# Optimization experiments

Hardware: AMD Instinct MI355X
Metric: run time of the kernel (lower is better)

## Reference

```python
import jax, jax.numpy as jnp
import numpy as np

H = 8  # n_heads

def setup_inputs() -> dict:
    key = jax.random.key(0)
    k1, k2, k3, k4, k5 = jax.random.split(key, 5)
    B, N, D = 4, 2048, 512
    x = jax.random.normal(k1, (B, N, D), dtype=jnp.float32)
    mask_flat = jax.random.randint(k2, (B, N), 0, 2).astype(bool)
    s = 1.0 / np.sqrt(D)
    Wq = jax.random.normal(k3, (D, D), dtype=jnp.float32) * s
    Wkv = jax.random.normal(k4, (D, 2 * D), dtype=jnp.float32) * s
    Wo = jax.random.normal(k5, (D, D), dtype=jnp.float32) * s
    return {"x": x, "mask_flat": mask_flat, "Wq": Wq, "Wkv": Wkv, "Wo": Wo}

def reference(x, mask_flat, Wq, Wkv, Wo):
    B, N, D = x.shape
    d = D // H
    scale = d ** -0.5
    kv = x @ Wkv                                   # (B,N,2D)
    k, v = jnp.split(kv, 2, axis=-1)
    q = x @ Wq                                     # (B,N,D)
    # (B,H,N,d)
    q = q.reshape(B, N, H, d).transpose(0, 2, 1, 3)
    k = k.reshape(B, N, H, d).transpose(0, 2, 1, 3)
    v = v.reshape(B, N, H, d).transpose(0, 2, 1, 3)
    attn = jax.nn.softmax(jnp.einsum('bhmd,bhnd->bhmn', q, k) * scale, axis=-1)
    res = jnp.einsum('bhmn,bhnd->bhmd', attn, v)   # (B,H,N,d)
    out = res.transpose(0, 2, 1, 3).reshape(B, N, D) @ Wo
    # non-masked query positions produce zero output (residual elsewhere keeps them)
    return jnp.where(mask_flat[..., None], out, 0.0)
```

## Files before the change

kernel.cpp:

```cpp
#include <hip/hip_runtime.h>

typedef __bf16 bf16x8 __attribute__((ext_vector_type(8)));
typedef float f32x4 __attribute__((ext_vector_type(4)));
typedef float f32x16 __attribute__((ext_vector_type(16)));
typedef unsigned short u16x8 __attribute__((ext_vector_type(8)));
typedef unsigned int u32x4 __attribute__((ext_vector_type(4)));
typedef int i32x2 __attribute__((ext_vector_type(2)));

__device__ inline unsigned short f2bf(float f) {
    __bf16 h = (__bf16)f;
    return __builtin_bit_cast(unsigned short, h);
}

__device__ inline unsigned int pkbf(float lo, float hi) {
    return (unsigned int)f2bf(lo) | ((unsigned int)f2bf(hi) << 16);
}

__device__ inline float fexp2(float x) {
#if __has_builtin(__builtin_amdgcn_exp2f)
    return __builtin_amdgcn_exp2f(x);
#else
    return exp2f(x);
#endif
}

__device__ inline f32x4 mfma16(u16x8 a, u16x8 b, f32x4 c) {
    return __builtin_amdgcn_mfma_f32_16x16x32_bf16(
        __builtin_bit_cast(bf16x8, a), __builtin_bit_cast(bf16x8, b), c, 0, 0, 0);
}

__device__ inline f32x16 mfma32(u16x8 a, u16x8 b, f32x16 c) {
    return __builtin_amdgcn_mfma_f32_32x32x16_bf16(
        __builtin_bit_cast(bf16x8, a), __builtin_bit_cast(bf16x8, b), c, 0, 0, 0);
}

__device__ inline i32x2 permswap(unsigned int a, unsigned int b, int hi) {
#if __has_builtin(__builtin_amdgcn_permlane32_swap)
    (void)hi;
    return __builtin_amdgcn_permlane32_swap((int)a, (int)b, false, false);
#else
    int pa_ = __shfl_xor((int)a, 32);
    int pb_ = __shfl_xor((int)b, 32);
    i32x2 r;
    r[0] = hi ? pb_ : (int)a;
    r[1] = hi ? (int)b : pa_;
    return r;
#endif
}

__device__ inline void gld_lds16(const unsigned short* gsrc, unsigned short* ldst) {
    __builtin_amdgcn_global_load_lds(
        (const __attribute__((address_space(1))) unsigned int*)gsrc,
        (__attribute__((address_space(3))) unsigned int*)ldst, 16, 0, 0);
}

#define WAIT_VM(n)                                          \
    asm volatile("s_waitcnt vmcnt(" #n ")" ::: "memory");   \
    __builtin_amdgcn_sched_barrier(0)
#define WAIT_LGKM0                                          \
    asm volatile("s_waitcnt lgkmcnt(0)" ::: "memory");      \
    __builtin_amdgcn_sched_barrier(0)
#define BARRIER                                             \
    __builtin_amdgcn_s_barrier();                           \
    __builtin_amdgcn_sched_barrier(0)

__global__ __launch_bounds__(256) void cvt_f32_bf16(const float* __restrict__ in,
                                                    unsigned short* __restrict__ out, long n) {
    long i = ((long)blockIdx.x * blockDim.x + threadIdx.x) * 4;
    if (i >= n) return;
    float4 v = *(const float4*)(in + i);
    ushort4 r;
    r.x = f2bf(v.x); r.y = f2bf(v.y); r.z = f2bf(v.z); r.w = f2bf(v.w);
    *(ushort4*)(out + i) = r;
}

__global__ __launch_bounds__(256) void transpose_cvt_tiled(const float* __restrict__ W,
                                                           unsigned short* __restrict__ Wt,
                                                           int K, int N, float scale) {
    __shared__ float tile[64][65];
    const int n0 = blockIdx.x * 64, k0 = blockIdx.y * 64;
    const int c = threadIdx.x & 63;
    const int r4 = threadIdx.x >> 6;
#pragma unroll
    for (int i = 0; i < 16; i++) {
        int r = r4 * 16 + i;
        tile[r][c] = W[(long)(k0 + r) * N + n0 + c];
    }
    __syncthreads();
#pragma unroll
    for (int i = 0; i < 16; i++) {
        int rr = r4 * 16 + i;
        Wt[(long)(n0 + rr) * K + k0 + c] = f2bf(tile[c][rr] * scale);
    }
}

__global__ __launch_bounds__(256) void scan_mask(const int* __restrict__ mask,
                                                 int* __restrict__ idx, int* __restrict__ cnt) {
    const int b = blockIdx.x;
    const int tid = threadIdx.x;
    __shared__ int wsum[4];
    int m[8]; int pc = 0;
#pragma unroll
    for (int k = 0; k < 8; k++) { m[k] = mask[b * 2048 + tid * 8 + k]; pc += (m[k] != 0); }
    int s = pc;
    const int lane = tid & 63;
    for (int off = 1; off < 64; off <<= 1) {
        int v = __shfl_up(s, off);
        if (lane >= off) s += v;
    }
    if (lane == 63) wsum[tid >> 6] = s;
    __syncthreads();
    int wbase = 0;
    for (int w = 0; w < (tid >> 6); w++) wbase += wsum[w];
    int run = wbase + s - pc;
#pragma unroll
    for (int k = 0; k < 8; k++) if (m[k]) idx[b * 2048 + (run++)] = tid * 8 + k;
    if (tid == 255) cnt[b] = wbase + s;
}

template<int WRITE_BF16, int MASKED>
__global__ __launch_bounds__(256) void gemm_bt(const unsigned short* __restrict__ A,
                                               const unsigned short* __restrict__ Bt,
                                               void* __restrict__ Cv,
                                               int M, int N, int K,
                                               const int* __restrict__ mask) {
    __shared__ unsigned short AsL[2][128 * 32];
    __shared__ unsigned short BsL[2][128 * 32];
    const int tid = threadIdx.x;
    const int lane = tid & 63;
    const int wid = tid >> 6;
    const int lg = lane >> 4, lr = lane & 15;
    const int wm = wid >> 1, wn = wid & 1;
    const long m0 = (long)blockIdx.y * 128, n0 = (long)blockIdx.x * 128;

    f32x4 acc[4][4] = {};

    const unsigned short* aS0 = A  + (m0 + (tid >> 2)) * K + (tid & 3) * 8;
    const unsigned short* aS1 = A  + (m0 + 64 + (tid >> 2)) * K + (tid & 3) * 8;
    const unsigned short* bS0 = Bt + (n0 + (tid >> 2)) * K + (tid & 3) * 8;
    const unsigned short* bS1 = Bt + (n0 + 64 + (tid >> 2)) * K + (tid & 3) * 8;

#define GSTAGE(bufi, k0v)                                    \
    {                                                        \
        gld_lds16(aS0 + (k0v), &AsL[bufi][wid * 512]);       \
        gld_lds16(aS1 + (k0v), &AsL[bufi][2048 + wid * 512]);\
        gld_lds16(bS0 + (k0v), &BsL[bufi][wid * 512]);       \
        gld_lds16(bS1 + (k0v), &BsL[bufi][2048 + wid * 512]);\
    }
#define GREAD(cur)                                                                    \
    {                                                                                 \
        _Pragma("unroll")                                                             \
        for (int i = 0; i < 4; i++) {                                                 \
            af[i]  = *(const u16x8*)&AsL[cur][(wm * 64 + i * 16 + lr) * 32 + lg * 8]; \
            bfr[i] = *(const u16x8*)&BsL[cur][(wn * 64 + i * 16 + lr) * 32 + lg * 8]; \
        }                                                                             \
    }
#define GMFMA                                                                  \
    {                                                                          \
        _Pragma("unroll")                                                      \
        for (int i = 0; i < 4; i++)                                            \
            _Pragma("unroll")                                                  \
            for (int j = 0; j < 4; j++)                                        \
                acc[i][j] = mfma16(af[i], bfr[j], acc[i][j]);                  \
    }

    const int nk = K >> 5;
    GSTAGE(0, 0);
    GSTAGE(1, 32);
    for (int t = 0; t < nk - 1; t++) {
        const int cur = t & 1;
        u16x8 af[4], bfr[4];
        WAIT_VM(4);
        BARRIER;
        GREAD(cur);
        WAIT_LGKM0;
        BARRIER;
        if (t < nk - 2) GSTAGE(cur, (t + 2) * 32);
        GMFMA;
    }
    {
        u16x8 af[4], bfr[4];
        WAIT_VM(0);
        BARRIER;
        GREAD((nk - 1) & 1);
        GMFMA;
    }
#undef GSTAGE
#undef GREAD
#undef GMFMA

#pragma unroll
    for (int i = 0; i < 4; i++)
#pragma unroll
        for (int j = 0; j < 4; j++)
#pragma unroll
            for (int r = 0; r < 4; r++) {
                long row = m0 + wm * 64 + i * 16 + lg * 4 + r;
                long col = n0 + wn * 64 + j * 16 + lr;
                float v = acc[i][j][r];
                if (MASKED) {
                    if (!mask[row]) v = 0.0f;
                    ((float*)Cv)[row * N + col] = v;
                } else if (WRITE_BF16) {
                    ((unsigned short*)Cv)[row * N + col] = f2bf(v);
                } else {
                    ((float*)Cv)[row * N + col] = v;
                }
            }
}

__global__ __launch_bounds__(256) void attn_kernel(const unsigned short* __restrict__ qk,
                                                   const unsigned short* __restrict__ vT,
                                                   unsigned short* __restrict__ res,
                                                   const int* __restrict__ idxm,
                                                   const int* __restrict__ cntm) {
    const int Nseq = 2048, LD = 1024;
    const long T = 8192;
    const int id = blockIdx.x;
    const int xcd = id & 7, jj = id >> 3;
    const int g = xcd + 8 * (jj & 3);
    const int qt = jj >> 2;
    const int b = g >> 3, h = g & 7;

    const int count = cntm[b];
    if (qt * 64 >= count) return;

    const int tid = threadIdx.x;
    const int wid = tid >> 6, lane = tid & 63;
    const int qL = lane & 31, hi = lane >> 5;
    const int qh = wid >> 1, kvh = wid & 1;

    __shared__ unsigned short LDSB[4][2][4096];
    unsigned short* myL = &LDSB[wid][0][0];

    const int i_q = qt * 64 + qh * 32 + qL;
    const int gi = idxm[b * 2048 + (i_q < count ? i_q : count - 1)];
    const long qrow = (long)b * Nseq + gi;
    u16x8 qf[4];
#pragma unroll
    for (int j = 0; j < 4; j++)
        qf[j] = *(const u16x8*)(qk + qrow * LD + h * 64 + 16 * j + 8 * hi);

    f32x16 oacc[2] = {};
    f32x16 lacc = {};
    u16x8 onesf;
#pragma unroll
    for (int e = 0; e < 8; e++) onesf[e] = 0x3F80;

    const int R0 = lane >> 3, p0 = lane & 7;
    const unsigned short* kS = qk + 512 + ((long)b * Nseq + kvh * 1024 + R0) * LD + h * 64
                               + ((p0 ^ R0) * 8);
    const int rV = lane >> 2, pV = lane & 3;
    const unsigned short* vS = vT + ((long)h * 64 + rV) * T + (long)b * Nseq + kvh * 1024
                               + ((pV ^ ((lane >> 3) & 3)) * 8);
    const int rsw = qL & 7;

#define STAGE(bufi)                                                          \
    {                                                                        \
        unsigned short* dK = myL + (bufi) * 4096;                            \
        _Pragma("unroll")                                                    \
        for (int i = 0; i < 4; i++)                                          \
            gld_lds16(kS + (long)i * 8 * LD, dK + i * 512);                  \
        _Pragma("unroll")                                                    \
        for (int i = 0; i < 4; i++)                                          \
            gld_lds16(vS + (long)i * 16 * T, dK + 2048 + i * 512);           \
        kS += 32L * LD; vS += 32;                                            \
    }

#define READ_KF(buf)                                                           \
    {                                                                          \
        _Pragma("unroll")                                                      \
        for (int j = 0; j < 4; j++)                                            \
            kf[j] = *(const u16x8*)&myL[(buf) * 4096 + qL * 64                 \
                                        + (((2 * j + hi) ^ rsw) * 8)];         \
    }
#define READ_VF(buf)                                                           \
    {                                                                          \
        _Pragma("unroll")                                                      \
        for (int db = 0; db < 2; db++)                                         \
            _Pragma("unroll")                                                  \
            for (int jk = 0; jk < 2; jk++)                                     \
                vf[db][jk] = *(const u16x8*)&myL[(buf) * 4096 + 2048           \
                                 + (db * 32 + qL) * 32                         \
                                 + (((2 * jk + hi) ^ ((qL >> 1) & 3)) * 8)];   \
    }

#define QKNEXT(SN)                                                             \
    {                                                                          \
        SN = (f32x16){};                                                       \
        _Pragma("unroll")                                                      \
        for (int j = 0; j < 4; j++) SN = mfma32(kf[j], qf[j], SN);             \
    }

#define PACK_PV(SC)                                                                    \
    {                                                                                  \
        unsigned int w[8];                                                             \
        _Pragma("unroll")                                                              \
        for (int i = 0; i < 8; i++)                                                    \
            w[i] = pkbf(fexp2(SC[2 * i]), fexp2(SC[2 * i + 1]));                       \
        u16x8 pa[2];                                                                   \
        _Pragma("unroll")                                                              \
        for (int hh = 0; hh < 2; hh++) {                                               \
            i32x2 ra = permswap(w[4 * hh + 0], w[4 * hh + 2], hi);                     \
            i32x2 rb = permswap(w[4 * hh + 1], w[4 * hh + 3], hi);                     \
            u32x4 fw;                                                                  \
            fw[0] = (unsigned)ra[0]; fw[1] = (unsigned)rb[0];                          \
            fw[2] = (unsigned)ra[1]; fw[3] = (unsigned)rb[1];                          \
            pa[hh] = __builtin_bit_cast(u16x8, fw);                                    \
        }                                                                              \
        _Pragma("unroll")                                                              \
        for (int jk = 0; jk < 2; jk++) {                                               \
            lacc = mfma32(pa[jk], onesf, lacc);                                        \
            oacc[0] = mfma32(pa[jk], vf[0][jk], oacc[0]);                              \
            oacc[1] = mfma32(pa[jk], vf[1][jk], oacc[1]);                              \
        }                                                                              \
    }

#define STEP(SC, SN, cur)                                                      \
    {                                                                          \
        WAIT_VM(4);                                                            \
        READ_VF(cur);                                                          \
        READ_KF(cur ^ 1);                                                      \
        WAIT_LGKM0;                                                            \
        STAGE(cur);                                                            \
        QKNEXT(SN);                                                            \
        PACK_PV(SC);                                                           \
    }

    u16x8 kf[4], vf[2][2];
    f32x16 sA, sB;

    STAGE(0);
    STAGE(1);
    WAIT_VM(12);
    READ_KF(0);
    WAIT_LGKM0;
    QKNEXT(sA);

    for (int t = 0; t < 30; t += 2) {
        STEP(sA, sB, 0);
        STEP(sB, sA, 1);
    }
    {
        WAIT_VM(4);
        READ_VF(0);
        READ_KF(1);
        WAIT_LGKM0;
        QKNEXT(sB);
        PACK_PV(sA);
    }
    {
        WAIT_VM(0);
        READ_VF(1);
        WAIT_LGKM0;
        PACK_PV(sB);
    }
#undef STAGE
#undef READ_KF
#undef READ_VF
#undef QKNEXT
#undef PACK_PV
#undef STEP

    __syncthreads();
    float* Ox = (float*)&LDSB[0][0][0];
    float* lX = Ox + 2 * 32 * 65;

    if (kvh == 1) {
#pragma unroll
        for (int reg = 0; reg < 16; reg++) {
            const int crow = (reg & 3) + 8 * (reg >> 2) + 4 * hi;
            Ox[qh * 2080 + crow * 65 + qL]      = oacc[0][reg];
            Ox[qh * 2080 + crow * 65 + 32 + qL] = oacc[1][reg];
            lX[qh * 32 + crow] = lacc[reg];
        }
    }
    __syncthreads();
    if (kvh == 0) {
#pragma unroll
        for (int reg = 0; reg < 16; reg++) {
            const int crow = (reg & 3) + 8 * (reg >> 2) + 4 * hi;
            const int row_c = qt * 64 + qh * 32 + crow;
            if (row_c < count) {
                float lt = lacc[reg] + lX[qh * 32 + crow];
                float linv = 1.0f / lt;
                float o0 = oacc[0][reg] + Ox[qh * 2080 + crow * 65 + qL];
                float o1 = oacc[1][reg] + Ox[qh * 2080 + crow * 65 + 32 + qL];
                const int orig = idxm[b * 2048 + row_c];
                long row = (long)b * Nseq + orig;
                res[row * 512 + h * 64 + qL]      = f2bf(o0 * linv);
                res[row * 512 + h * 64 + 32 + qL] = f2bf(o1 * linv);
            }
        }
    }
}

extern "C" void kernel_launch(void* const* d_in, const int* in_sizes, int n_in,
                              void* d_out, int out_size, void* d_ws, size_t ws_size,
                              hipStream_t stream) {
    const float* x   = (const float*)d_in[0];
    const int* mask  = (const int*)d_in[1];
    const float* Wq  = (const float*)d_in[2];
    const float* Wkv = (const float*)d_in[3];
    const float* Wo  = (const float*)d_in[4];
    float* out = (float*)d_out;

    const int Nseq = 2048, D = 512;
    const long T = 8192;
    const float QSCALE = 0.125f * 1.4426950408889634f;

    unsigned short* ws    = (unsigned short*)d_ws;
    unsigned short* xb    = ws;
    unsigned short* WqkvT = xb    + T * D;
    unsigned short* WoT   = WqkvT + 1536L * 512;
    unsigned short* qkb   = WoT   + 512L * 512;
    unsigned short* vTb   = qkb   + T * 1024;
    unsigned short* resb  = vTb   + 512L * T;
    int* idxb = (int*)(resb + T * 512);
    int* cntb = idxb + 4 * 2048;

    cvt_f32_bf16<<<(int)(T * D / 1024), 256, 0, stream>>>(x, xb, T * D);
    transpose_cvt_tiled<<<dim3(8, 8),  256, 0, stream>>>(Wq,  WqkvT,              D, 512,  QSCALE);
    transpose_cvt_tiled<<<dim3(16, 8), 256, 0, stream>>>(Wkv, WqkvT + 512L * 512, D, 1024, 1.0f);
    transpose_cvt_tiled<<<dim3(8, 8),  256, 0, stream>>>(Wo,  WoT,                D, 512,  1.0f);
    scan_mask<<<4, 256, 0, stream>>>(mask, idxb, cntb);

    gemm_bt<1, 0><<<dim3(8, 64), 256, 0, stream>>>(xb, WqkvT, qkb, T, 1024, D, nullptr);
    gemm_bt<1, 0><<<dim3(64, 4), 256, 0, stream>>>(WqkvT + 1024L * 512, xb, vTb, D, T, D, nullptr);

    attn_kernel<<<1024, 256, 0, stream>>>(qkb, vTb, resb, idxb, cntb);

    gemm_bt<0, 1><<<dim3(4, 64), 256, 0, stream>>>(resb, WoT, out, T, D, D, mask);
}
```

Before: 107.4 us.

## Share K/V tiles across query-half waves in attention and merge weight prep launches

The attention kernel now has the two waves that handle different query halves share one LDS K/V tile per kv-half. Each wave stages a 32-row slice of a 64-key block cooperatively, and s_barrier calls synchronise the shared buffers. Each step now processes 64 keys, half as many iterations as before, which reduces redundant global-to-LDS traffic for K and V. In exchange it adds block-wide barriers and needs more registers for the doubled score and fragment arrays. Separately, the three weight transpose/convert launches are merged into one 3D-grid kernel to cut launch overhead.

After: 99.89 us. -7.0%, faster.

```diff
diff --git a/kernel.cpp b/kernel.cpp
--- a/kernel.cpp
+++ b/kernel.cpp
@@ -74,10 +74,20 @@
     *(ushort4*)(out + i) = r;
 }
 
-__global__ __launch_bounds__(256) void transpose_cvt_tiled(const float* __restrict__ W,
-                                                           unsigned short* __restrict__ Wt,
-                                                           int K, int N, float scale) {
+__global__ __launch_bounds__(256) void prep_weights(const float* __restrict__ Wq,
+                                                    const float* __restrict__ Wkv,
+                                                    const float* __restrict__ Wo,
+                                                    unsigned short* __restrict__ WqkvT,
+                                                    unsigned short* __restrict__ WoT,
+                                                    float qscale) {
     __shared__ float tile[64][65];
+    const int z = blockIdx.z;
+    if (z != 1 && blockIdx.x >= 8) return;
+    const float* W = (z == 0) ? Wq : (z == 1) ? Wkv : Wo;
+    unsigned short* Wt = (z == 0) ? WqkvT : (z == 1) ? (WqkvT + 512L * 512) : WoT;
+    const int N = (z == 1) ? 1024 : 512;
+    const float scale = (z == 0) ? qscale : 1.0f;
+    const int K = 512;
     const int n0 = blockIdx.x * 64, k0 = blockIdx.y * 64;
     const int c = threadIdx.x & 63;
     const int r4 = threadIdx.x >> 6;
@@ -230,8 +240,7 @@
     const int qL = lane & 31, hi = lane >> 5;
     const int qh = wid >> 1, kvh = wid & 1;
 
-    __shared__ unsigned short LDSB[4][2][4096];
-    unsigned short* myL = &LDSB[wid][0][0];
+    __shared__ unsigned short LDSB[2][2][8192];
 
     const int i_q = qt * 64 + qh * 32 + qL;
     const int gi = idxm[b * 2048 + (i_q < count ? i_q : count - 1)];
@@ -247,110 +256,124 @@
 #pragma unroll
     for (int e = 0; e < 8; e++) onesf[e] = 0x3F80;
 
-    const int R0 = lane >> 3, p0 = lane & 7;
-    const unsigned short* kS = qk + 512 + ((long)b * Nseq + kvh * 1024 + R0) * LD + h * 64
-                               + ((p0 ^ R0) * 8);
-    const int rV = lane >> 2, pV = lane & 3;
-    const unsigned short* vS = vT + ((long)h * 64 + rV) * T + (long)b * Nseq + kvh * 1024
-                               + ((pV ^ ((lane >> 3) & 3)) * 8);
+    const int Rs = lane >> 3, p0 = lane & 7;
+    const int psw = (p0 ^ Rs) * 8;
+    const unsigned short* kS = qk + 512 + ((long)b * Nseq + kvh * 1024 + 32 * qh + Rs) * LD
+                               + h * 64 + psw;
+    const unsigned short* vS = vT + ((long)h * 64 + 32 * qh + Rs) * T + (long)b * Nseq
+                               + kvh * 1024 + psw;
     const int rsw = qL & 7;
 
-#define STAGE(bufi)                                                          \
-    {                                                                        \
-        unsigned short* dK = myL + (bufi) * 4096;                            \
-        _Pragma("unroll")                                                    \
-        for (int i = 0; i < 4; i++)                                          \
-            gld_lds16(kS + (long)i * 8 * LD, dK + i * 512);                  \
-        _Pragma("unroll")                                                    \
-        for (int i = 0; i < 4; i++)                                          \
-            gld_lds16(vS + (long)i * 16 * T, dK + 2048 + i * 512);           \
-        kS += 32L * LD; vS += 32;                                            \
-    }
-
-#define READ_KF(buf)                                                           \
-    {                                                                          \
-        _Pragma("unroll")                                                      \
-        for (int j = 0; j < 4; j++)                                            \
-            kf[j] = *(const u16x8*)&myL[(buf) * 4096 + qL * 64                 \
-                                        + (((2 * j + hi) ^ rsw) * 8)];         \
-    }
-#define READ_VF(buf)                                                           \
-    {                                                                          \
-        _Pragma("unroll")                                                      \
-        for (int db = 0; db < 2; db++)                                         \
-            _Pragma("unroll")                                                  \
-            for (int jk = 0; jk < 2; jk++)                                     \
-                vf[db][jk] = *(const u16x8*)&myL[(buf) * 4096 + 2048           \
-                                 + (db * 32 + qL) * 32                         \
-                                 + (((2 * jk + hi) ^ ((qL >> 1) & 3)) * 8)];   \
-    }
-
-#define QKNEXT(SN)                                                             \
-    {                                                                          \
-        SN = (f32x16){};                                                       \
-        _Pragma("unroll")                                                      \
-        for (int j = 0; j < 4; j++) SN = mfma32(kf[j], qf[j], SN);             \
+#define STAGE(bufi)                                                             \
+    {                                                                           \
+        _Pragma("unroll")                                                       \
+        for (int i = 0; i < 4; i++)                                             \
+            gld_lds16(kS + (long)i * 8 * LD,                                    \
+                      &LDSB[kvh][bufi][(qh * 4 + i) * 512]);                    \
+        _Pragma("unroll")                                                       \
+        for (int i = 0; i < 4; i++)                                             \
+            gld_lds16(vS + (long)i * 8 * T,                                     \
+                      &LDSB[kvh][bufi][4096 + (qh * 4 + i) * 512]);             \
+        kS += 64L * LD; vS += 64;                                               \
+    }
+
+#define READ_KF(buf)                                                            \
+    {                                                                           \
+        _Pragma("unroll")                                                       \
+        for (int kvb = 0; kvb < 2; kvb++)                                       \
+            _Pragma("unroll")                                                   \
+            for (int j = 0; j < 4; j++)                                         \
+                kf[kvb][j] = *(const u16x8*)&LDSB[kvh][buf][(kvb * 32 + qL) * 64\
+                                             + (((2 * j + hi) ^ rsw) * 8)];     \
+    }
+#define READ_VF(buf)                                                            \
+    {                                                                           \
+        _Pragma("unroll")                                                       \
+        for (int db = 0; db < 2; db++)                                          \
+            _Pragma("unroll")                                                   \
+            for (int jk = 0; jk < 4; jk++)                                      \
+                vf[db][jk] = *(const u16x8*)&LDSB[kvh][buf][4096                \
+                                 + (db * 32 + qL) * 64                          \
+                                 + (((2 * jk + hi) ^ rsw) * 8)];                \
+    }
+
+#define QKNEXT(SN)                                                              \
+    {                                                                           \
+        SN[0] = (f32x16){}; SN[1] = (f32x16){};                                 \
+        _Pragma("unroll")                                                       \
+        for (int j = 0; j < 4; j++) {                                           \
+            SN[0] = mfma32(kf[0][j], qf[j], SN[0]);                             \
+            SN[1] = mfma32(kf[1][j], qf[j], SN[1]);                             \
+        }                                                                       \
     }
 
 #define PACK_PV(SC)                                                                    \
     {                                                                                  \
-        unsigned int w[8];                                                             \
+        u16x8 pa[4];                                                                   \
         _Pragma("unroll")                                                              \
-        for (int i = 0; i < 8; i++)                                                    \
-            w[i] = pkbf(fexp2(SC[2 * i]), fexp2(SC[2 * i + 1]));                       \
-        u16x8 pa[2];                                                                   \
-        _Pragma("unroll")                                                              \
-        for (int hh = 0; hh < 2; hh++) {                                               \
-            i32x2 ra = permswap(w[4 * hh + 0], w[4 * hh + 2], hi);                     \
-            i32x2 rb = permswap(w[4 * hh + 1], w[4 * hh + 3], hi);                     \
-            u32x4 fw;                                                                  \
-            fw[0] = (unsigned)ra[0]; fw[1] = (unsigned)rb[0];                          \
-            fw[2] = (unsigned)ra[1]; fw[3] = (unsigned)rb[1];                          \
-            pa[hh] = __builtin_bit_cast(u16x8, fw);                                    \
+        for (int kvb = 0; kvb < 2; kvb++) {                                            \
+            unsigned int w[8];                                                         \
+            _Pragma("unroll")                                                          \
+            for (int i = 0; i < 8; i++)                                                \
+                w[i] = pkbf(fexp2(SC[kvb][2 * i]), fexp2(SC[kvb][2 * i + 1]));         \
+            _Pragma("unroll")                                                          \
+            for (int hh = 0; hh < 2; hh++) {                                           \
+                i32x2 ra = permswap(w[4 * hh + 0], w[4 * hh + 2], hi);                 \
+                i32x2 rb = permswap(w[4 * hh + 1], w[4 * hh + 3], hi);                 \
+                u32x4 fw;                                                              \
+                fw[0] = (unsigned)ra[0]; fw[1] = (unsigned)rb[0];                      \
+                fw[2] = (unsigned)ra[1]; fw[3] = (unsigned)rb[1];                      \
+                pa[kvb * 2 + hh] = __builtin_bit_cast(u16x8, fw);                      \
+            }                                                                          \
         }                                                                              \
         _Pragma("unroll")                                                              \
-        for (int jk = 0; jk < 2; jk++) {                                               \
+        for (int jk = 0; jk < 4; jk++) {                                               \
             lacc = mfma32(pa[jk], onesf, lacc);                                        \
             oacc[0] = mfma32(pa[jk], vf[0][jk], oacc[0]);                              \
             oacc[1] = mfma32(pa[jk], vf[1][jk], oacc[1]);                              \
         }                                                                              \
     }
 
-#define STEP(SC, SN, cur)                                                      \
-    {                                                                          \
-        WAIT_VM(4);                                                            \
-        READ_VF(cur);                                                          \
-        READ_KF(cur ^ 1);                                                      \
-        WAIT_LGKM0;                                                            \
-        STAGE(cur);                                                            \
-        QKNEXT(SN);                                                            \
-        PACK_PV(SC);                                                           \
-    }
-
-    u16x8 kf[4], vf[2][2];
-    f32x16 sA, sB;
+#define STEP(SC, SN, cur)                                                       \
+    {                                                                           \
+        WAIT_VM(4);          \
+        BARRIER;                                             \
+        READ_KF(cur ^ 1);                                                       \
+        READ_VF(cur);                                                           \
+        WAIT_LGKM0;                                                             \
+        BARRIER;                \
+        STAGE(cur);                                                             \
+        QKNEXT(SN);                                                             \
+        PACK_PV(SC);                                                            \
+    }
+
+    u16x8 kf[2][4], vf[2][4];
+    f32x16 sA[2], sB[2];
 
     STAGE(0);
     STAGE(1);
     WAIT_VM(12);
+    BARRIER;
     READ_KF(0);
     WAIT_LGKM0;
     QKNEXT(sA);
 
-    for (int t = 0; t < 30; t += 2) {
+    for (int t = 0; t < 14; t += 2) {
         STEP(sA, sB, 0);
         STEP(sB, sA, 1);
     }
     {
         WAIT_VM(4);
+        BARRIER;
+        READ_KF(1);
         READ_VF(0);
-        READ_KF(1);
         WAIT_LGKM0;
         QKNEXT(sB);
         PACK_PV(sA);
     }
     {
         WAIT_VM(0);
+        BARRIER;
         READ_VF(1);
         WAIT_LGKM0;
         PACK_PV(sB);
@@ -420,9 +443,7 @@
     int* cntb = idxb + 4 * 2048;
 
     cvt_f32_bf16<<<(int)(T * D / 1024), 256, 0, stream>>>(x, xb, T * D);
-    transpose_cvt_tiled<<<dim3(8, 8),  256, 0, stream>>>(Wq,  WqkvT,              D, 512,  QSCALE);
-    transpose_cvt_tiled<<<dim3(16, 8), 256, 0, stream>>>(Wkv, WqkvT + 512L * 512, D, 1024, 1.0f);
-    transpose_cvt_tiled<<<dim3(8, 8),  256, 0, stream>>>(Wo,  WoT,                D, 512,  1.0f);
+    prep_weights<<<dim3(16, 8, 3), 256, 0, stream>>>(Wq, Wkv, Wo, WqkvT, WoT, QSCALE);
     scan_mask<<<4, 256, 0, stream>>>(mask, idxb, cntb);
 
     gemm_bt<1, 0><<<dim3(8, 64), 256, 0, stream>>>(xb, WqkvT, qkb, T, 1024, D, nullptr);
```

## Merge weight prep launches and shrink attention blocks to 32 queries

Applied to the files above, without the earlier changes.

Combines the three weight transpose/convert launches into one 3D-grid kernel to cut launch overhead. Restructures attention so each block handles 32 query rows with 2 waves (split KV halves) instead of 64 rows with 4 waves, doubling the grid. This spreads the masked workload more finely over the CUs, at the cost of each K/V tile being loaded for fewer queries, so global and LDS traffic per query rises.

Result: faster. 101.8 us (-5.1%).

```diff
diff --git a/kernel.cpp b/kernel.cpp
--- a/kernel.cpp
+++ b/kernel.cpp
@@ -74,10 +74,20 @@
     *(ushort4*)(out + i) = r;
 }
 
-__global__ __launch_bounds__(256) void transpose_cvt_tiled(const float* __restrict__ W,
-                                                           unsigned short* __restrict__ Wt,
-                                                           int K, int N, float scale) {
+__global__ __launch_bounds__(256) void prep_weights(const float* __restrict__ Wq,
+                                                    const float* __restrict__ Wkv,
+                                                    const float* __restrict__ Wo,
+                                                    unsigned short* __restrict__ WqkvT,
+                                                    unsigned short* __restrict__ WoT,
+                                                    float qscale) {
     __shared__ float tile[64][65];
+    const int z = blockIdx.z;
+    if (z != 1 && blockIdx.x >= 8) return;
+    const float* W = (z == 0) ? Wq : (z == 1) ? Wkv : Wo;
+    unsigned short* Wt = (z == 0) ? WqkvT : (z == 1) ? (WqkvT + 512L * 512) : WoT;
+    const int N = (z == 1) ? 1024 : 512;
+    const float scale = (z == 0) ? qscale : 1.0f;
+    const int K = 512;
     const int n0 = blockIdx.x * 64, k0 = blockIdx.y * 64;
     const int c = threadIdx.x & 63;
     const int r4 = threadIdx.x >> 6;
@@ -209,7 +219,7 @@
             }
 }
 
-__global__ __launch_bounds__(256) void attn_kernel(const unsigned short* __restrict__ qk,
+__global__ __launch_bounds__(128) void attn_kernel(const unsigned short* __restrict__ qk,
                                                    const unsigned short* __restrict__ vT,
                                                    unsigned short* __restrict__ res,
                                                    const int* __restrict__ idxm,
@@ -223,17 +233,17 @@
     const int b = g >> 3, h = g & 7;
 
     const int count = cntm[b];
-    if (qt * 64 >= count) return;
+    if (qt * 32 >= count) return;
 
     const int tid = threadIdx.x;
     const int wid = tid >> 6, lane = tid & 63;
     const int qL = lane & 31, hi = lane >> 5;
-    const int qh = wid >> 1, kvh = wid & 1;
-
-    __shared__ unsigned short LDSB[4][2][4096];
-    unsigned short* myL = &LDSB[wid][0][0];
-
-    const int i_q = qt * 64 + qh * 32 + qL;
+    const int kvh = wid;
+
+    __shared__ unsigned short LDSB[2][2][4096];
+    unsigned short* myL = &LDSB[kvh][0][0];
+
+    const int i_q = qt * 32 + qL;
     const int gi = idxm[b * 2048 + (i_q < count ? i_q : count - 1)];
     const long qrow = (long)b * Nseq + gi;
     u16x8 qf[4];
@@ -364,15 +374,15 @@
 
     __syncthreads();
     float* Ox = (float*)&LDSB[0][0][0];
-    float* lX = Ox + 2 * 32 * 65;
+    float* lX = Ox + 32 * 65;
 
     if (kvh == 1) {
 #pragma unroll
         for (int reg = 0; reg < 16; reg++) {
             const int crow = (reg & 3) + 8 * (reg >> 2) + 4 * hi;
-            Ox[qh * 2080 + crow * 65 + qL]      = oacc[0][reg];
-            Ox[qh * 2080 + crow * 65 + 32 + qL] = oacc[1][reg];
-            lX[qh * 32 + crow] = lacc[reg];
+            Ox[crow * 65 + qL]      = oacc[0][reg];
+            Ox[crow * 65 + 32 + qL] = oacc[1][reg];
+            lX[crow] = lacc[reg];
         }
     }
     __syncthreads();
@@ -380,12 +390,12 @@
 #pragma unroll
         for (int reg = 0; reg < 16; reg++) {
             const int crow = (reg & 3) + 8 * (reg >> 2) + 4 * hi;
-            const int row_c = qt * 64 + qh * 32 + crow;
+            const int row_c = qt * 32 + crow;
             if (row_c < count) {
-                float lt = lacc[reg] + lX[qh * 32 + crow];
+                float lt = lacc[reg] + lX[crow];
                 float linv = 1.0f / lt;
-                float o0 = oacc[0][reg] + Ox[qh * 2080 + crow * 65 + qL];
-                float o1 = oacc[1][reg] + Ox[qh * 2080 + crow * 65 + 32 + qL];
+                float o0 = oacc[0][reg] + Ox[crow * 65 + qL];
+                float o1 = oacc[1][reg] + Ox[crow * 65 + 32 + qL];
                 const int orig = idxm[b * 2048 + row_c];
                 long row = (long)b * Nseq + orig;
                 res[row * 512 + h * 64 + qL]      = f2bf(o0 * linv);
@@ -420,15 +430,13 @@
     int* cntb = idxb + 4 * 2048;
 
     cvt_f32_bf16<<<(int)(T * D / 1024), 256, 0, stream>>>(x, xb, T * D);
-    transpose_cvt_tiled<<<dim3(8, 8),  256, 0, stream>>>(Wq,  WqkvT,              D, 512,  QSCALE);
-    transpose_cvt_tiled<<<dim3(16, 8), 256, 0, stream>>>(Wkv, WqkvT + 512L * 512, D, 1024, 1.0f);
-    transpose_cvt_tiled<<<dim3(8, 8),  256, 0, stream>>>(Wo,  WoT,                D, 512,  1.0f);
+    prep_weights<<<dim3(16, 8, 3), 256, 0, stream>>>(Wq, Wkv, Wo, WqkvT, WoT, QSCALE);
     scan_mask<<<4, 256, 0, stream>>>(mask, idxb, cntb);
 
     gemm_bt<1, 0><<<dim3(8, 64), 256, 0, stream>>>(xb, WqkvT, qkb, T, 1024, D, nullptr);
     gemm_bt<1, 0><<<dim3(64, 4), 256, 0, stream>>>(WqkvT + 1024L * 512, xb, vTb, D, T, D, nullptr);
 
-    attn_kernel<<<1024, 256, 0, stream>>>(qkb, vTb, resb, idxb, cntb);
+    attn_kernel<<<2048, 128, 0, stream>>>(qkb, vTb, resb, idxb, cntb);
 
     gemm_bt<0, 1><<<dim3(4, 64), 256, 0, stream>>>(resb, WoT, out, T, D, D, mask);
 }
```
